# Performance work log

Measured on AMD Instinct MI355X. Metric: run time of the kernel, lower is better.

Reference implementation:

```python
import jax, jax.numpy as jnp
import numpy as np

NHID = 768
H = 128        # LSTM hidden per direction
NHEADS = 6
NDIR = 12      # 6 heads x 2 directions; first 6 = forward, last 6 = backward
DFF = 4 * NHID
CAT = 2 * H * NHEADS  # 1536


def setup_inputs() -> dict:
    key = jax.random.key(0)
    ks = jax.random.split(key, 12)
    s = 0.05
    return {
        "embeddings": jax.random.normal(ks[0], (16, 512, NHID), jnp.float32),
        # stacked LSTM params; gate order i,f,g,o as in PyTorch
        "W_ih": jax.random.normal(ks[1], (NDIR, 4 * H, NHID), jnp.float32) * s,
        "W_hh": jax.random.normal(ks[2], (NDIR, 4 * H, H), jnp.float32) * s,
        "b_ih": jax.random.normal(ks[3], (NDIR, 4 * H), jnp.float32) * s,
        "b_hh": jax.random.normal(ks[4], (NDIR, 4 * H), jnp.float32) * s,
        "W_int": jax.random.normal(ks[5], (DFF, CAT), jnp.float32) * s,
        "b_int": jax.random.normal(ks[6], (DFF,), jnp.float32) * s,
        "W_out": jax.random.normal(ks[7], (NHID, DFF), jnp.float32) * s,
        "b_out": jax.random.normal(ks[8], (NHID,), jnp.float32) * s,
        "gamma": jnp.ones((NHID,), jnp.float32),
        "beta": jnp.zeros((NHID,), jnp.float32),
    }


def _multi_bilstm(x, W_ih, W_hh, b_ih, b_hh):
    # x: [B,S,D] -> concat of 6 bidirectional LSTM outputs [B,S,1536]
    B, S, _ = x.shape
    # input projections for all 12 directions at once: [12,B,S,4H]
    xp = jnp.einsum('bsd,kgd->kbsg', x, W_ih) + (b_ih + b_hh)[:, None, None, :]
    # reverse time for the 6 backward directions
    xp = jnp.concatenate([xp[:NHEADS], xp[NHEADS:, :, ::-1]], axis=0)
    xs = jnp.moveaxis(xp, 2, 0)  # [S,12,B,4H]

    def step(carry, z_x):
        h, c = carry  # each [12,B,H]
        z = z_x + jnp.einsum('kbh,kgh->kbg', h, W_hh)
        i, f, g, o = jnp.split(z, 4, axis=-1)
        c = jax.nn.sigmoid(f) * c + jax.nn.sigmoid(i) * jnp.tanh(g)
        h = jax.nn.sigmoid(o) * jnp.tanh(c)
        return (h, c), h

    init = (jnp.zeros((NDIR, B, H), x.dtype), jnp.zeros((NDIR, B, H), x.dtype))
    _, ys = jax.lax.scan(step, init, xs)        # [S,12,B,H]
    ys = jnp.moveaxis(ys, 0, 2)                 # [12,B,S,H]
    ys = jnp.concatenate([ys[:NHEADS], ys[NHEADS:, :, ::-1]], axis=0)
    # per-head layout: head0_fwd, head0_bwd, head1_fwd, ... (matches torch.cat of per-LSTM outputs)
    ys = ys.reshape(2, NHEADS, B, S, H).transpose(2, 3, 1, 0, 4)
    return ys.reshape(B, S, CAT)


def reference(embeddings, W_ih, W_hh, b_ih, b_hh, W_int, b_int, W_out, b_out, gamma, beta):
    cat = _multi_bilstm(embeddings, W_ih, W_hh, b_ih, b_hh)
    inter = jax.nn.gelu(cat @ W_int.T + b_int, approximate=False)
    proj = inter @ W_out.T + b_out
    res = embeddings + proj  # dropout is identity (p=0 / eval)
    mu = jnp.mean(res, axis=-1, keepdims=True)
    var = jnp.mean(jnp.square(res - mu), axis=-1, keepdims=True)
    return (res - mu) * jax.lax.rsqrt(var + 1e-5) * gamma + beta
```

## Files before the change

### kernel.cpp

```cpp
#include <hip/hip_runtime.h>

typedef __attribute__((ext_vector_type(4))) float f32x4;
typedef __attribute__((ext_vector_type(8))) short short8;
typedef unsigned short u16;
typedef unsigned int u32;

__device__ __forceinline__ u16 f2bf(float f){
  u32 x = __float_as_uint(f);
  u32 r = x + 0x7fffu + ((x >> 16) & 1u);
  return (u16)(r >> 16);
}
__device__ __forceinline__ float bf2f32(u32 u){ return __uint_as_float(u << 16); }

__device__ __forceinline__ void gld_lds16(const u16* g, u16* l){
  __builtin_amdgcn_global_load_lds((const __attribute__((address_space(1))) void*)g,
                                   (__attribute__((address_space(3))) void*)l, 16, 0, 0);
}

__device__ __forceinline__ f32x4 mfma16(short8 a, short8 b, f32x4 c){
  return __builtin_amdgcn_mfma_f32_16x16x32_bf16(a, b, c, 0, 0, 0);
}

__device__ __forceinline__ float sigf(float x){
  return __builtin_amdgcn_rcpf(1.0f + __expf(-x));
}
__device__ __forceinline__ float tanhf_(float x){
  float e = __expf(2.0f * x);
  return 1.0f - 2.0f * __builtin_amdgcn_rcpf(e + 1.0f);
}

__global__ __launch_bounds__(256) void k_castall(const float* __restrict__ s0, const float* __restrict__ s1,
                          const float* __restrict__ s2, const float* __restrict__ s3,
                          u16* __restrict__ d0, u16* __restrict__ d1, u16* __restrict__ d2,
                          u16* __restrict__ d3)
{
  int i = blockIdx.x * 256 + threadIdx.x;
  const float* s; u16* d; int off;
  if (i < 1572864)      { s = s0; d = d0; off = i; }
  else if (i < 1769472) { s = s1; d = d1; off = i - 1572864; }
  else if (i < 2949120) { s = s2; d = d2; off = i - 1769472; }
  else                  { s = s3; d = d3; off = i - 2949120; }
  float4 v = ((const float4*)s)[off];
  ushort4 o; o.x=f2bf(v.x); o.y=f2bf(v.y); o.z=f2bf(v.z); o.w=f2bf(v.w);
  ((ushort4*)d)[off] = o;
}

__global__ __launch_bounds__(192) void k_permw(const float* __restrict__ wih, u16* __restrict__ dst)
{
  int np = blockIdx.x;
  int d = np >> 9, r = np & 511;
  int src = d*512 + (r & 3)*128 + (r >> 2);
  float4 v = ((const float4*)(wih + (size_t)src*768))[threadIdx.x];
  ushort4 o; o.x=f2bf(v.x); o.y=f2bf(v.y); o.z=f2bf(v.z); o.w=f2bf(v.w);
  ((ushort4*)(dst + (size_t)np*768))[threadIdx.x] = o;
}

template<int MODE>
__global__ __launch_bounds__(512) void k_gemm3(
    const u16* __restrict__ A, const u16* __restrict__ B,
    void* __restrict__ C, void* __restrict__ C2,
    const float* __restrict__ bias1, const float* __restrict__ bias2,
    int M, int N, int K, int lda)
{
  __shared__ __align__(16) u16 lA[2][256*64];
  __shared__ __align__(16) u16 lB[3][192*64];
  int nwg = gridDim.x;
  int bid = blockIdx.x;
  int half = 0;
  if (MODE == 2){
    int h2 = nwg >> 1;
    half = (bid >= h2) ? 1 : 0;
    bid -= half ? h2 : 0;
    nwg = h2;
  }
  int koff = half * K;
  int q = nwg >> 3;
  int swz = (bid & 7) * q + (bid >> 3);
  int nbn = N / 192;
  int grp = nbn << 3;
  int gid = swz / grp, rem = swz % grp;
  int bm = (gid << 3) + (rem & 7), bn = rem >> 3;
  int tid = threadIdx.x, lane = tid & 63;
  int wv = tid >> 6;
  int wm = wv & 1, wn = wv >> 1;
  int l15 = lane & 15, lhi = lane >> 4;
  const u16* Ag = A + (size_t)(bm << 8) * lda + koff;
  const u16* Bg = B + (size_t)(bn * 192) * lda + koff;

  int srA[4], slA[4];
  #pragma unroll
  for (int i = 0; i < 4; ++i){
    int c = i*512 + tid;
    srA[i] = c >> 3;
    slA[i] = (((c & 7) ^ (srA[i] & 7)) << 3);
  }
  int srB[3], slB[3];
  #pragma unroll
  for (int i = 0; i < 3; ++i){
    int c = i*512 + tid;
    srB[i] = c >> 3;
    slB[i] = (((c & 7) ^ (srB[i] & 7)) << 3);
  }
  int axr = l15 & 7;
  int aoff0 = (wm*128 + l15)*64 + ((lhi    ) ^ axr)*8;
  int aoff1 = (wm*128 + l15)*64 + ((lhi + 4) ^ axr)*8;
  int boff0 = (wn*48  + l15)*64 + ((lhi    ) ^ axr)*8;
  int boff1 = (wn*48  + l15)*64 + ((lhi + 4) ^ axr)*8;

  f32x4 acc[8][3];
  #pragma unroll
  for (int i = 0; i < 8; ++i)
    #pragma unroll
    for (int j = 0; j < 3; ++j)
      acc[i][j] = (f32x4){0.f,0.f,0.f,0.f};

  int NT = K >> 6;

#define STAGE_A(TT)                                                            \
  { int ko = (TT) << 6; u16* dA = lA[(TT) & 1];                                \
    _Pragma("unroll")                                                          \
    for (int i = 0; i < 4; ++i)                                                \
      gld_lds16(Ag + (size_t)srA[i]*lda + ko + slA[i], &dA[(i*512+tid)*8]); }
#define STAGE_B(TT)                                                            \
  { int ko = (TT) << 6; u16* dB = lB[(TT) % 3];                                \
    _Pragma("unroll")                                                          \
    for (int i = 0; i < 3; ++i)                                                \
      gld_lds16(Bg + (size_t)srB[i]*lda + ko + slB[i], &dB[(i*512+tid)*8]); }

  STAGE_A(0)
  STAGE_B(0)
  STAGE_B(1)
  asm volatile("s_waitcnt vmcnt(3)" ::: "memory");
  __builtin_amdgcn_s_barrier();

  for (int t = 0; t < NT; ++t){
    const u16* sA = lA[t & 1];
    const u16* sB = lB[t % 3];
    short8 bf[3][2];
    #pragma unroll
    for (int p = 0; p < 4; ++p){
      if (p == 0){
        #pragma unroll
        for (int ni = 0; ni < 3; ++ni){
          bf[ni][0] = *(const short8*)&sB[boff0 + ni*1024];
          bf[ni][1] = *(const short8*)&sB[boff1 + ni*1024];
        }
      }
      short8 a00 = *(const short8*)&sA[aoff0 + (2*p)*1024];
      short8 a01 = *(const short8*)&sA[aoff1 + (2*p)*1024];
      short8 a10 = *(const short8*)&sA[aoff0 + (2*p+1)*1024];
      short8 a11 = *(const short8*)&sA[aoff1 + (2*p+1)*1024];
      if (p == 0 && t + 1 < NT){ STAGE_A(t+1) }
      if (p == 1 && t + 2 < NT){ STAGE_B(t+2) }
      asm volatile("s_barrier" ::: "memory");
      __builtin_amdgcn_s_setprio(1);
      #pragma unroll
      for (int ni = 0; ni < 3; ++ni){
        acc[2*p  ][ni] = mfma16(a00, bf[ni][0], acc[2*p  ][ni]);
        acc[2*p  ][ni] = mfma16(a01, bf[ni][1], acc[2*p  ][ni]);
        acc[2*p+1][ni] = mfma16(a10, bf[ni][0], acc[2*p+1][ni]);
        acc[2*p+1][ni] = mfma16(a11, bf[ni][1], acc[2*p+1][ni]);
      }
      __builtin_amdgcn_s_setprio(0);
      if (p == 3){
        if (t + 2 < NT){
          asm volatile("s_waitcnt vmcnt(3)" ::: "memory");
        } else if (t + 1 < NT){
          asm volatile("s_waitcnt vmcnt(0)" ::: "memory");
        }
      }
      asm volatile("s_barrier" ::: "memory");
    }
  }
#undef STAGE_A
#undef STAGE_B

  #pragma unroll
  for (int ni = 0; ni < 3; ++ni){
    int n = bn*192 + wn*48 + ni*16 + l15;
    float bs;
    if (MODE == 0){
      int d = n >> 9, r = n & 511;
      int src = d*512 + (r & 3)*128 + (r >> 2);
      bs = bias1[src] + bias2[src];
    } else {
      bs = bias1[n];
    }
    #pragma unroll
    for (int mi = 0; mi < 8; ++mi){
      #pragma unroll
      for (int r = 0; r < 4; ++r){
        int m = (bm << 8) + wm*128 + mi*16 + lhi*4 + r;
        float v = acc[mi][ni][r];
        if (MODE == 2){
          if (!half) v += bs;
          ((float*)(half ? C2 : C))[(size_t)m * N + n] = v;
        } else {
          v += bs;
          if (MODE == 1)
            v = 0.5f * v * (1.0f + erff(v * 0.70710678118f));
          ((u16*)C)[(size_t)m * N + n] = f2bf(v);
        }
      }
    }
  }
}

__global__ __launch_bounds__(512) void k_scan(const u16* __restrict__ whh, const u16* __restrict__ xp,
                       u16* __restrict__ cat)
{
  __shared__ __align__(16) u16 hb[2][4*144];
  int bid = blockIdx.x;
  int d = bid >> 2, bg = bid & 3;
  int tid = threadIdx.x, lane = tid & 63, w = tid >> 6;
  int l15 = lane & 15, lhi = lane >> 4;

  u16* hbf = (u16*)hb;
  for (int i = tid; i < 2*4*144; i += 512) hbf[i] = 0;

  short8 wf[4][4];
  #pragma unroll
  for (int g = 0; g < 4; ++g)
    #pragma unroll
    for (int kk = 0; kk < 4; ++kk)
      wf[g][kk] = *(const short8*)(whh + ((size_t)d*512 + g*128 + w*16 + l15)*128 + kk*32 + lhi*8);

  int b = bg*4 + lhi;
  int dim = w*16 + l15;
  bool fwd = (d < 6);
  const u16* zbase = xp + (size_t)b*512*6144 + d*512 + dim*4;

  ushort4 Z[4];
  #pragma unroll
  for (int j = 0; j < 4; ++j){
    int s = fwd ? j : 511 - j;
    Z[j] = *(const ushort4*)(zbase + (size_t)s*6144);
  }

  f32x4 a0={0.f,0.f,0.f,0.f}, a1=a0, a2=a0, a3=a0;
  float cr = 0.f;
  int head = fwd ? d : d - 6;
  int posoff = fwd ? 0 : 128;
  size_t catlane = (size_t)b*512*1536 + head*256 + posoff + dim;
  int catoff = fwd ? 0 : 511*1536;
  int catstep = fwd ? 1536 : -1536;

  int hrd = (l15 >> 2)*144 + lhi*8;
  int hwr = lhi*144 + dim;

  __syncthreads();

#define SCAN_STEP(T, RB, WB, S)                                                \
  {                                                                            \
    short8 hf0 = *(const short8*)&hb[RB][hrd + 0*32];                          \
    short8 hf1 = *(const short8*)&hb[RB][hrd + 1*32];                          \
    short8 hf2 = *(const short8*)&hb[RB][hrd + 2*32];                          \
    short8 hf3 = *(const short8*)&hb[RB][hrd + 3*32];                          \
    a0[0] = bf2f32((u32)Z[S].x); a1[0] = bf2f32((u32)Z[S].y);                  \
    a2[0] = bf2f32((u32)Z[S].z); a3[0] = bf2f32((u32)Z[S].w);                  \
    int t4 = (T) + 4; if (t4 > 511) t4 = 511;                                  \
    int s4 = fwd ? t4 : 511 - t4;                                              \
    Z[S] = *(const ushort4*)(zbase + (size_t)s4*6144);                         \
    a2 = mfma16(hf0, wf[2][0], a2); a0 = mfma16(hf0, wf[0][0], a0);            \
    a1 = mfma16(hf0, wf[1][0], a1); a3 = mfma16(hf0, wf[3][0], a3);            \
    a2 = mfma16(hf1, wf[2][1], a2); a0 = mfma16(hf1, wf[0][1], a0);            \
    a1 = mfma16(hf1, wf[1][1], a1); a3 = mfma16(hf1, wf[3][1], a3);            \
    a2 = mfma16(hf2, wf[2][2], a2); a0 = mfma16(hf2, wf[0][2], a0);            \
    a1 = mfma16(hf2, wf[1][2], a1); a3 = mfma16(hf2, wf[3][2], a3);            \
    a2 = mfma16(hf3, wf[2][3], a2); a0 = mfma16(hf3, wf[0][3], a0);            \
    a1 = mfma16(hf3, wf[1][3], a1); a3 = mfma16(hf3, wf[3][3], a3);            \
    float tg = tanhf_(a2[0]);                                                  \
    float fi = sigf(a0[0]), ff = sigf(a1[0]), fo = sigf(a3[0]);                \
    cr = ff*cr + fi*tg;                                                        \
    float hv = fo * tanhf_(cr);                                                \
    u32 hp32;                                                                  \
    asm("v_cvt_pk_bf16_f32 %0, %1, %2" : "=v"(hp32) : "v"(hv), "v"(hv));       \
    u16 hp = (u16)hp32;                                                        \
    hb[WB][hwr] = hp;                                                          \
    cat[catlane + catoff] = hp;                                                \
    catoff += catstep;                                                         \
    asm volatile("s_waitcnt lgkmcnt(0)" ::: "memory");                         \
    __builtin_amdgcn_s_barrier();                                              \
  }

  for (int t = 0; t < 512; t += 4){
    SCAN_STEP(t,   0, 1, 0)
    SCAN_STEP(t+1, 1, 0, 1)
    SCAN_STEP(t+2, 0, 1, 2)
    SCAN_STEP(t+3, 1, 0, 3)
  }
#undef SCAN_STEP
}

__global__ __launch_bounds__(256) void k_ln(const float* __restrict__ emb, const float* __restrict__ p0,
                     const float* __restrict__ p1,
                     const float* __restrict__ gamma, const float* __restrict__ beta,
                     float* __restrict__ out)
{
  int row = blockIdx.x, tid = threadIdx.x;
  const float* pe = emb + (size_t)row * 768;
  const float* pa = p0 + (size_t)row * 768;
  const float* pb = p1 + (size_t)row * 768;
  float v0 = pe[tid]     + pa[tid]     + pb[tid];
  float v1 = pe[tid+256] + pa[tid+256] + pb[tid+256];
  float v2 = pe[tid+512] + pa[tid+512] + pb[tid+512];
  float s = v0+v1+v2, s2 = v0*v0+v1*v1+v2*v2;
  #pragma unroll
  for (int o = 32; o > 0; o >>= 1){ s += __shfl_down(s, o); s2 += __shfl_down(s2, o); }
  __shared__ float rs[4], rq[4];
  int wv = tid >> 6;
  if ((tid & 63) == 0){ rs[wv] = s; rq[wv] = s2; }
  __syncthreads();
  s = rs[0]+rs[1]+rs[2]+rs[3];
  s2 = rq[0]+rq[1]+rq[2]+rq[3];
  float mu = s * (1.0f/768.0f);
  float var = s2 * (1.0f/768.0f) - mu*mu;
  float rr = rsqrtf(var + 1e-5f);
  float* po = out + (size_t)row * 768;
  po[tid]     = (v0-mu)*rr*gamma[tid]     + beta[tid];
  po[tid+256] = (v1-mu)*rr*gamma[tid+256] + beta[tid+256];
  po[tid+512] = (v2-mu)*rr*gamma[tid+512] + beta[tid+512];
}

extern "C" void kernel_launch(void* const* d_in, const int* in_sizes, int n_in,
                              void* d_out, int out_size, void* d_ws, size_t ws_size,
                              hipStream_t stream)
{
  const float* emb   = (const float*)d_in[0];
  const float* W_ih  = (const float*)d_in[1];
  const float* W_hh  = (const float*)d_in[2];
  const float* b_ih  = (const float*)d_in[3];
  const float* b_hh  = (const float*)d_in[4];
  const float* W_int = (const float*)d_in[5];
  const float* b_int = (const float*)d_in[6];
  const float* W_out = (const float*)d_in[7];
  const float* b_out = (const float*)d_in[8];
  const float* gamma = (const float*)d_in[9];
  const float* beta  = (const float*)d_in[10];
  float* out = (float*)d_out;

  char* ws = (char*)d_ws;
  u16* embb  = (u16*)(ws + 0);
  u16* wihb  = (u16*)(ws + 12582912);
  u16* whhb  = (u16*)(ws + 22020096);
  u16* wintb = (u16*)(ws + 23592960);
  u16* woutb = (u16*)(ws + 33030144);
  u16* catb  = (u16*)(ws + 37748736);
  float* proj1=(float*)(ws + 37748736);
  u16* xp    = (u16*)(ws + 62914560);
  u16* interb= (u16*)(ws + 62914560);
  float* proj0=(float*)(ws + 113246208);

  hipLaunchKernelGGL(k_castall, dim3(13824), dim3(256), 0, stream,
                     emb, W_hh, W_int, W_out, embb, whhb, wintb, woutb);
  hipLaunchKernelGGL(k_permw, dim3(6144), dim3(192), 0, stream, W_ih, wihb);

  hipLaunchKernelGGL((k_gemm3<0>), dim3(1024), dim3(512), 0, stream,
                     embb, wihb, (void*)xp, nullptr, b_ih, b_hh, 8192, 6144, 768, 768);
  hipLaunchKernelGGL(k_scan, dim3(48), dim3(512), 0, stream, whhb, xp, catb);
  hipLaunchKernelGGL((k_gemm3<1>), dim3(512), dim3(512), 0, stream,
                     catb, wintb, (void*)interb, nullptr, b_int, nullptr, 8192, 3072, 1536, 1536);
  hipLaunchKernelGGL((k_gemm3<2>), dim3(256), dim3(512), 0, stream,
                     interb, woutb, (void*)proj0, (void*)proj1, b_out, nullptr, 8192, 768, 1536, 3072);
  hipLaunchKernelGGL(k_ln, dim3(8192), dim3(256), 0, stream, emb, proj0, proj1, gamma, beta, out);
}
```

Baseline: 503.3 us.

## Make GEMMs persistent over multiple N-tiles with continuous cross-tile prefetch

Turns the GEMM kernel into a semi-persistent one. Each workgroup handles TPW consecutive N-tiles of 192 columns for the same 256-row A block, and the load pipeline runs straight across tile boundaries. The epilogue moves inside the loop and clears the accumulators after each tile's store. This cuts the grid to 256 workgroups (one wave on the CUs) and removes per-tile pipeline ramp-up and tail costs. The risk is that the epilogue stores now stall the pipeline mid-stream, the grouped-M swizzle for L2 reuse is dropped, and the modulo/divide address math adds cost.

```diff
diff --git a/kernel.cpp b/kernel.cpp
--- a/kernel.cpp
+++ b/kernel.cpp
@@ -55,8 +55,8 @@
   ((ushort4*)(dst + (size_t)np*768))[threadIdx.x] = o;
 }
 
-template<int MODE>
-__global__ __launch_bounds__(512) void k_gemm3(
+template<int MODE, int TPW>
+__global__ __launch_bounds__(512) void k_gemmp(
     const u16* __restrict__ A, const u16* __restrict__ B,
     void* __restrict__ C, void* __restrict__ C2,
     const float* __restrict__ bias1, const float* __restrict__ bias2,
@@ -76,16 +76,15 @@
   int koff = half * K;
   int q = nwg >> 3;
   int swz = (bid & 7) * q + (bid >> 3);
-  int nbn = N / 192;
-  int grp = nbn << 3;
-  int gid = swz / grp, rem = swz % grp;
-  int bm = (gid << 3) + (rem & 7), bn = rem >> 3;
+  int nbng = N / (192 * TPW);
+  int bm = swz / nbng, bng = swz % nbng;
   int tid = threadIdx.x, lane = tid & 63;
   int wv = tid >> 6;
   int wm = wv & 1, wn = wv >> 1;
   int l15 = lane & 15, lhi = lane >> 4;
   const u16* Ag = A + (size_t)(bm << 8) * lda + koff;
-  const u16* Bg = B + (size_t)(bn * 192) * lda + koff;
+  const u16* Bg0 = B + (size_t)(bng * TPW) * 192 * lda + koff;
+  size_t bstep = (size_t)192 * lda;
 
   int srA[4], slA[4];
   #pragma unroll
@@ -115,17 +114,20 @@
       acc[i][j] = (f32x4){0.f,0.f,0.f,0.f};
 
   int NT = K >> 6;
-
-#define STAGE_A(TT)                                                            \
-  { int ko = (TT) << 6; u16* dA = lA[(TT) & 1];                                \
+  int TOT = NT * TPW;
+
+#define STAGE_A(SS)                                                            \
+  { int ss_ = (SS); int ko = (ss_ % NT) << 6; u16* dA = lA[ss_ & 1];           \
     _Pragma("unroll")                                                          \
     for (int i = 0; i < 4; ++i)                                                \
       gld_lds16(Ag + (size_t)srA[i]*lda + ko + slA[i], &dA[(i*512+tid)*8]); }
-#define STAGE_B(TT)                                                            \
-  { int ko = (TT) << 6; u16* dB = lB[(TT) % 3];                                \
+#define STAGE_B(SS)                                                            \
+  { int ss_ = (SS); int ko = (ss_ % NT) << 6;                                  \
+    const u16* Bb = Bg0 + (size_t)(ss_ / NT) * bstep;                          \
+    u16* dB = lB[ss_ % 3];                                                     \
     _Pragma("unroll")                                                          \
     for (int i = 0; i < 3; ++i)                                                \
-      gld_lds16(Bg + (size_t)srB[i]*lda + ko + slB[i], &dB[(i*512+tid)*8]); }
+      gld_lds16(Bb + (size_t)srB[i]*lda + ko + slB[i], &dB[(i*512+tid)*8]); }
 
   STAGE_A(0)
   STAGE_B(0)
@@ -133,9 +135,10 @@
   asm volatile("s_waitcnt vmcnt(3)" ::: "memory");
   __builtin_amdgcn_s_barrier();
 
-  for (int t = 0; t < NT; ++t){
-    const u16* sA = lA[t & 1];
-    const u16* sB = lB[t % 3];
+  int kt = 0, tile = 0;
+  for (int tt = 0; tt < TOT; ++tt){
+    const u16* sA = lA[tt & 1];
+    const u16* sB = lB[tt % 3];
     short8 bf[3][2];
     #pragma unroll
     for (int p = 0; p < 4; ++p){
@@ -150,8 +153,8 @@
       short8 a01 = *(const short8*)&sA[aoff1 + (2*p)*1024];
       short8 a10 = *(const short8*)&sA[aoff0 + (2*p+1)*1024];
       short8 a11 = *(const short8*)&sA[aoff1 + (2*p+1)*1024];
-      if (p == 0 && t + 1 < NT){ STAGE_A(t+1) }
-      if (p == 1 && t + 2 < NT){ STAGE_B(t+2) }
+      if (p == 0 && tt + 1 < TOT){ STAGE_A(tt+1) }
+      if (p == 1 && tt + 2 < TOT){ STAGE_B(tt+2) }
       asm volatile("s_barrier" ::: "memory");
       __builtin_amdgcn_s_setprio(1);
       #pragma unroll
@@ -163,47 +166,54 @@
       }
       __builtin_amdgcn_s_setprio(0);
       if (p == 3){
-        if (t + 2 < NT){
+        if (tt + 2 < TOT){
           asm volatile("s_waitcnt vmcnt(3)" ::: "memory");
-        } else if (t + 1 < NT){
+        } else if (tt + 1 < TOT){
           asm volatile("s_waitcnt vmcnt(0)" ::: "memory");
         }
       }
       asm volatile("s_barrier" ::: "memory");
     }
+
+    if (kt == NT - 1){
+      int bnbase = (bng * TPW + tile) * 192;
+      #pragma unroll
+      for (int ni = 0; ni < 3; ++ni){
+        int n = bnbase + wn*48 + ni*16 + l15;
+        float bs;
+        if (MODE == 0){
+          int d = n >> 9, r = n & 511;
+          int src = d*512 + (r & 3)*128 + (r >> 2);
+          bs = bias1[src] + bias2[src];
+        } else {
+          bs = bias1[n];
+        }
+        #pragma unroll
+        for (int mi = 0; mi < 8; ++mi){
+          #pragma unroll
+          for (int r = 0; r < 4; ++r){
+            int m = (bm << 8) + wm*128 + mi*16 + lhi*4 + r;
+            float v = acc[mi][ni][r];
+            if (MODE == 2){
+              if (!half) v += bs;
+              ((float*)(half ? C2 : C))[(size_t)m * N + n] = v;
+            } else {
+              v += bs;
+              if (MODE == 1)
+                v = 0.5f * v * (1.0f + erff(v * 0.70710678118f));
+              ((u16*)C)[(size_t)m * N + n] = f2bf(v);
+            }
+            acc[mi][ni][r] = 0.f;
+          }
+        }
+      }
+      ++tile; kt = 0;
+    } else {
+      ++kt;
+    }
   }
 #undef STAGE_A
 #undef STAGE_B
-
-  #pragma unroll
-  for (int ni = 0; ni < 3; ++ni){
-    int n = bn*192 + wn*48 + ni*16 + l15;
-    float bs;
-    if (MODE == 0){
-      int d = n >> 9, r = n & 511;
-      int src = d*512 + (r & 3)*128 + (r >> 2);
-      bs = bias1[src] + bias2[src];
-    } else {
-      bs = bias1[n];
-    }
-    #pragma unroll
-    for (int mi = 0; mi < 8; ++mi){
-      #pragma unroll
-      for (int r = 0; r < 4; ++r){
-        int m = (bm << 8) + wm*128 + mi*16 + lhi*4 + r;
-        float v = acc[mi][ni][r];
-        if (MODE == 2){
-          if (!half) v += bs;
-          ((float*)(half ? C2 : C))[(size_t)m * N + n] = v;
-        } else {
-          v += bs;
-          if (MODE == 1)
-            v = 0.5f * v * (1.0f + erff(v * 0.70710678118f));
-          ((u16*)C)[(size_t)m * N + n] = f2bf(v);
-        }
-      }
-    }
-  }
 }
 
 __global__ __launch_bounds__(512) void k_scan(const u16* __restrict__ whh, const u16* __restrict__ xp,
@@ -355,12 +365,12 @@
                      emb, W_hh, W_int, W_out, embb, whhb, wintb, woutb);
   hipLaunchKernelGGL(k_permw, dim3(6144), dim3(192), 0, stream, W_ih, wihb);
 
-  hipLaunchKernelGGL((k_gemm3<0>), dim3(1024), dim3(512), 0, stream,
+  hipLaunchKernelGGL((k_gemmp<0,4>), dim3(256), dim3(512), 0, stream,
                      embb, wihb, (void*)xp, nullptr, b_ih, b_hh, 8192, 6144, 768, 768);
   hipLaunchKernelGGL(k_scan, dim3(48), dim3(512), 0, stream, whhb, xp, catb);
-  hipLaunchKernelGGL((k_gemm3<1>), dim3(512), dim3(512), 0, stream,
+  hipLaunchKernelGGL((k_gemmp<1,2>), dim3(256), dim3(512), 0, stream,
                      catb, wintb, (void*)interb, nullptr, b_int, nullptr, 8192, 3072, 1536, 1536);
-  hipLaunchKernelGGL((k_gemm3<2>), dim3(256), dim3(512), 0, stream,
+  hipLaunchKernelGGL((k_gemmp<2,1>), dim3(256), dim3(512), 0, stream,
                      interb, woutb, (void*)proj0, (void*)proj1, b_out, nullptr, 8192, 768, 1536, 3072);
   hipLaunchKernelGGL(k_ln, dim3(8192), dim3(256), 0, stream, emb, proj0, proj1, gamma, beta, out);
 }
```

After: 499.3 us. Within noise of the previous version (-0.8%).
